# Kernel optimization log

Hardware: AMD Instinct MI355X
Metric: run time of the kernel (lower is better)

Reference implementation:

```python
import jax, jax.numpy as jnp
import numpy as np

HEADS = 16
DIM_HEAD = 64
NEG_INF = -1e30


def _rope_cos_sin(seq_len, dim_head, dtype):
    inv_freq = 1.0 / (10000.0 ** (jnp.arange(0, dim_head, 2, dtype=jnp.float32) / dim_head))
    t = jnp.arange(seq_len, dtype=jnp.float32)
    freqs = jnp.einsum('i,j->ij', t, inv_freq)          # [n, dh/2]
    emb = jnp.concatenate([freqs, freqs], axis=-1)       # [n, dh]
    return jnp.cos(emb).astype(dtype), jnp.sin(emb).astype(dtype)


def _rotate_half(x):
    x1, x2 = jnp.split(x, 2, axis=-1)
    return jnp.concatenate([-x2, x1], axis=-1)


def setup_inputs() -> dict:
    key = jax.random.key(0)
    k1, k2, k3 = jax.random.split(key, 3)
    dim = HEADS * DIM_HEAD  # 1024
    x = jax.random.normal(k1, (2, 2048, dim), dtype=jnp.float32)
    w_qkv = jax.random.normal(k2, (dim, 3 * dim), dtype=jnp.float32) * (dim ** -0.5)
    w_out = jax.random.normal(k3, (dim, dim), dtype=jnp.float32) * (dim ** -0.5)
    return {"x": x, "w_qkv": w_qkv, "w_out": w_out}


def reference(x, w_qkv, w_out):
    b, n, d = x.shape
    h, dh = HEADS, DIM_HEAD
    scale = dh ** -0.5

    qkv = x @ w_qkv                                      # [b, n, 3*h*dh]
    q, k, v = jnp.split(qkv, 3, axis=-1)
    reshape = lambda t: t.reshape(b, n, h, dh).transpose(0, 2, 1, 3)  # b h n dh
    q, k, v = reshape(q), reshape(k), reshape(v)

    cos, sin = _rope_cos_sin(n, dh, x.dtype)
    cos = cos[None, None, :, :]
    sin = sin[None, None, :, :]
    q = q * cos + _rotate_half(q) * sin
    k = k * cos + _rotate_half(k) * sin

    scores = jnp.einsum('bhid,bhjd->bhij', q, k) * scale  # [b, h, n, n]
    causal = jnp.triu(jnp.ones((n, n), dtype=bool), k=1)
    scores = jnp.where(causal[None, None, :, :], NEG_INF, scores)
    attn = jax.nn.softmax(scores, axis=-1)

    out = jnp.einsum('bhij,bhjd->bhid', attn, v)          # [b, h, n, dh]
    out = out.transpose(0, 2, 1, 3).reshape(b, n, h * dh)
    return out @ w_out
```

## Files before the change

kernel.cpp:

```cpp
#include <hip/hip_runtime.h>

#define SEQ 2048
#define NH 16
#define DH 64
#define DMODEL 1024
#define NQKV 3072

typedef __attribute__((ext_vector_type(8))) short bf16x8;
typedef __attribute__((ext_vector_type(4))) short bf16x4;
typedef __attribute__((ext_vector_type(4))) float f32x4;

#define GLOAD16(src, dst)                                                              \
  __builtin_amdgcn_global_load_lds((const __attribute__((address_space(1))) void*)(src), \
                                   (__attribute__((address_space(3))) void*)(dst), 16, 0, 0)

__device__ __forceinline__ unsigned short f2bf(float f) {
  union { float f; unsigned u; } v; v.f = f;
  unsigned r = v.u + 0x7FFFu + ((v.u >> 16) & 1u);
  return (unsigned short)(r >> 16);
}

__device__ __forceinline__ unsigned pkbf(float a, float b) {
  unsigned r;
  asm("v_cvt_pk_bf16_f32 %0, %1, %2" : "=v"(r) : "v"(a), "v"(b));
  return r;
}

__device__ __forceinline__ void transw_body(const float* __restrict__ in,
                                            unsigned short* __restrict__ out,
                                            int K, int N, int k0, int n0, int tid,
                                            float (*Ts)[65]) {
#pragma unroll
  for (int p = 0; p < 4; ++p) {
    int id = p * 256 + tid;
    int r = id >> 4, c4 = (id & 15) * 4;
    const f32x4 v = *reinterpret_cast<const f32x4*>(&in[(size_t)(k0 + r) * N + n0 + c4]);
    Ts[r][c4] = v[0]; Ts[r][c4 + 1] = v[1]; Ts[r][c4 + 2] = v[2]; Ts[r][c4 + 3] = v[3];
  }
  __syncthreads();
#pragma unroll
  for (int p = 0; p < 2; ++p) {
    int id = p * 256 + tid;
    int n = id >> 3, k8 = (id & 7) * 8;
    unsigned short tmp[8];
#pragma unroll
    for (int i = 0; i < 8; ++i) tmp[i] = f2bf(Ts[k8 + i][n]);
    *reinterpret_cast<bf16x8*>(&out[(size_t)(n0 + n) * K + k0 + k8]) =
        *reinterpret_cast<bf16x8*>(tmp);
  }
}

__global__ __launch_bounds__(256) void prep_kernel(
    const float* __restrict__ x, const float* __restrict__ w_qkv,
    const float* __restrict__ w_out, unsigned short* __restrict__ Xb,
    unsigned short* __restrict__ WqkvT, unsigned short* __restrict__ WoutT,
    float* __restrict__ cost, float* __restrict__ sint) {
  __shared__ float Ts[64][65];
  const int tid = threadIdx.x;
  const int id = blockIdx.x;
  if (id < 2048) {
    int idx = id * 256 + tid;
    const f32x4 v0 = *reinterpret_cast<const f32x4*>(&x[(size_t)idx * 8]);
    const f32x4 v1 = *reinterpret_cast<const f32x4*>(&x[(size_t)idx * 8 + 4]);
    bf16x8 o;
    o[0] = (short)f2bf(v0[0]); o[1] = (short)f2bf(v0[1]);
    o[2] = (short)f2bf(v0[2]); o[3] = (short)f2bf(v0[3]);
    o[4] = (short)f2bf(v1[0]); o[5] = (short)f2bf(v1[1]);
    o[6] = (short)f2bf(v1[2]); o[7] = (short)f2bf(v1[3]);
    *reinterpret_cast<bf16x8*>(&Xb[(size_t)idx * 8]) = o;
  } else if (id < 2816) {
    int t = id - 2048;
    transw_body(w_qkv, WqkvT, DMODEL, NQKV, (t & 15) * 64, (t >> 4) * 64, tid, Ts);
  } else if (id < 3072) {
    int t = id - 2816;
    transw_body(w_out, WoutT, DMODEL, DMODEL, (t & 15) * 64, (t >> 4) * 64, tid, Ts);
  } else {
    int idx = (id - 3072) * 256 + tid;
    int t = idx >> 5, j = idx & 31;
    float inv = powf(10000.0f, -(float)(2 * j) / 64.0f);
    float a = (float)t * inv;
    cost[idx] = cosf(a);
    sint[idx] = sinf(a);
  }
}

__global__ __launch_bounds__(256) void gemm_qkv_kernel(
    const unsigned short* __restrict__ Xb, const unsigned short* __restrict__ BT,
    unsigned short* __restrict__ Qb, unsigned short* __restrict__ Kb,
    unsigned short* __restrict__ Vtg,
    const float* __restrict__ cost, const float* __restrict__ sint) {
  __shared__ unsigned short As[3][4096];
  __shared__ unsigned short Bs[3][4096];

  const int tid = threadIdx.x;
  const int lane = tid & 63;
  const int w = tid >> 6;
  const int lam = lane & 15;
  const int g = lane >> 4;
  const int wr = w >> 1, wc = w & 1;
  const int rowBase = blockIdx.x * 128;
  const int colBase = blockIdx.y * 128;

  f32x4 acc[4][4];
#pragma unroll
  for (int m = 0; m < 4; ++m)
#pragma unroll
    for (int n = 0; n < 4; ++n) acc[m][n] = (f32x4){0.f, 0.f, 0.f, 0.f};

#define GSTAGE(buf, kk0)                                                               \
  {                                                                                    \
    _Pragma("unroll") for (int c = 0; c < 2; ++c) {                                    \
      int ch = c * 256 + w * 64 + lane;                                                \
      int row = ch >> 2, q = ch & 3;                                                   \
      GLOAD16(Xb + (size_t)(rowBase + row) * DMODEL + (kk0) + ((q ^ (row & 3)) * 8),   \
              &As[buf][0] + (c * 256 + w * 64) * 8);                                   \
      GLOAD16(BT + (size_t)(colBase + row) * DMODEL + (kk0) + ((q ^ (row & 3)) * 8),   \
              &Bs[buf][0] + (c * 256 + w * 64) * 8);                                   \
    }                                                                                  \
  }

  GSTAGE(0, 0);
  GSTAGE(1, 32);

  for (int kb = 0; kb < 32; ++kb) {
    if (kb + 2 < 32) {
      GSTAGE((kb + 2) % 3, (kb + 2) * 32);
      asm volatile("s_waitcnt vmcnt(8)" ::: "memory");
    } else if (kb + 1 < 32) {
      asm volatile("s_waitcnt vmcnt(4)" ::: "memory");
    } else {
      asm volatile("s_waitcnt vmcnt(0)" ::: "memory");
    }
    __builtin_amdgcn_s_barrier();
    const int cb = kb % 3;
    bf16x8 a[4], b[4];
    const int sw = (g ^ (lam & 3)) * 8;
#pragma unroll
    for (int m = 0; m < 4; ++m)
      a[m] = *reinterpret_cast<bf16x8*>(&As[cb][(wr * 64 + m * 16 + lam) * 32 + sw]);
#pragma unroll
    for (int n = 0; n < 4; ++n)
      b[n] = *reinterpret_cast<bf16x8*>(&Bs[cb][(wc * 64 + n * 16 + lam) * 32 + sw]);
    __builtin_amdgcn_s_setprio(1);
#pragma unroll
    for (int m = 0; m < 4; ++m)
#pragma unroll
      for (int n = 0; n < 4; ++n)
        acc[m][n] = __builtin_amdgcn_mfma_f32_16x16x32_bf16(a[m], b[n], acc[m][n], 0, 0, 0);
    __builtin_amdgcn_s_setprio(0);
    asm volatile("s_waitcnt lgkmcnt(0)" ::: "memory");
    __builtin_amdgcn_s_barrier();
  }
#undef GSTAGE

  const int mat = blockIdx.y >> 3;
  if (mat < 2) {
    unsigned short* dst = mat ? Kb : Qb;
    const float sc = mat ? 1.0f : 0.125f;
    const int h = ((colBase & 1023) + wc * 64) >> 6;
#pragma unroll
    for (int m = 0; m < 4; ++m) {
#pragma unroll
      for (int r = 0; r < 4; ++r) {
        int row = rowBase + wr * 64 + m * 16 + g * 4 + r;
        int bi = row >> 11, t = row & 2047;
        unsigned short* out = &dst[(size_t)((bi * NH + h) * SEQ + t) * DH];
#pragma unroll
        for (int n = 0; n < 2; ++n) {
          int j = n * 16 + lam;
          float c = cost[t * 32 + j], s = sint[t * 32 + j];
          float x0 = acc[m][n][r], x1 = acc[m][n + 2][r];
          out[j] = f2bf((x0 * c - x1 * s) * sc);
          out[j + 32] = f2bf((x1 * c + x0 * s) * sc);
        }
      }
    }
  } else {
    unsigned short (*Vbuf)[44] = reinterpret_cast<unsigned short(*)[44]>(&As[0][0]);
    const int b = rowBase >> 11, t0 = rowBase & 2047;
#pragma unroll
    for (int cc = 0; cc < 4; ++cc) {
      __syncthreads();
      if (wc == (cc >> 1)) {
        const int n0 = (cc & 1) * 2;
#pragma unroll
        for (int m = 0; m < 4; ++m)
#pragma unroll
          for (int r = 0; r < 4; ++r)
#pragma unroll
            for (int n2 = 0; n2 < 2; ++n2)
              Vbuf[wr * 64 + m * 16 + g * 4 + r][n2 * 16 + lam] = f2bf(acc[m][n0 + n2][r]);
      }
      __syncthreads();
      const int colq0 = colBase - 2048 + cc * 32;
#pragma unroll
      for (int p2 = 0; p2 < 2; ++p2) {
        int ch = p2 * 256 + tid;
        int d = ch & 31, tq = (ch >> 5) * 8;
        unsigned short tmp[8];
#pragma unroll
        for (int i = 0; i < 8; ++i) tmp[i] = Vbuf[tq + i][d];
        int col = colq0 + d;
        int h = col >> 6, dd = col & 63;
        *reinterpret_cast<bf16x8*>(&Vtg[((size_t)(b * NH + h) * DH + dd) * SEQ + t0 + tq]) =
            *reinterpret_cast<bf16x8*>(tmp);
      }
    }
  }
}

__global__ __launch_bounds__(256) void attn_kernel(
    const unsigned short* __restrict__ Qb, const unsigned short* __restrict__ Kb,
    const unsigned short* __restrict__ Vtg, unsigned short* __restrict__ Ob) {
  __shared__ unsigned short Ks[2][8192];
  __shared__ unsigned short Vs[2][8192];
  __shared__ unsigned short Ps[4][2048];

  const int tid = threadIdx.x;
  const int lane = tid & 63;
  const int w = tid >> 6;
  const int lam = lane & 15;
  const int g = lane >> 4;
  const int bh = blockIdx.x;
  const int p = blockIdx.y;
  const int qtA = p, qtB = 31 - p;
  const int nA = (p >> 1) + 1;
  const int nB = ((31 - p) >> 1) + 1;
  const int nT = nA + nB;
  const int ql = w * 16 + lam;

  const unsigned short* kallbase = Kb + (size_t)bh * SEQ * DH;
  const unsigned short* vallbase = Vtg + (size_t)bh * DH * SEQ;

  bf16x8 qb0, qb1;
  f32x4 oacc[4], sa0[4], sa1[4];
  float mr, lr;

#define LOADQ(qt)                                                                     \
  {                                                                                   \
    const unsigned short* qrow = Qb + ((size_t)bh * SEQ + (qt) * 64 + w * 16 + lam) * DH; \
    qb0 = *reinterpret_cast<const bf16x8*>(&qrow[g * 8]);                             \
    qb1 = *reinterpret_cast<const bf16x8*>(&qrow[g * 8 + 32]);                        \
  }
#define RESET_STATE()                                                                 \
  {                                                                                   \
    _Pragma("unroll") for (int f = 0; f < 4; ++f) oacc[f] = (f32x4){0.f, 0.f, 0.f, 0.f}; \
    mr = -1e30f; lr = 0.f;                                                            \
  }
#define STAGE(buf, jt)                                                                \
  {                                                                                   \
    const unsigned short* kb2 = kallbase + (size_t)(jt) * 128 * DH;                   \
    const unsigned short* vb2 = vallbase + (size_t)(jt) * 128;                        \
    _Pragma("unroll") for (int c = 0; c < 4; ++c) {                                   \
      int id = c * 256 + w * 64 + lane;                                               \
      int kr = id >> 3, kq = id & 7;                                                  \
      GLOAD16(kb2 + kr * DH + ((kq ^ (kr & 7)) * 8), &Ks[buf][0] + id * 8);           \
      int vr = id >> 4, vq = id & 15;                                                 \
      GLOAD16(vb2 + (size_t)vr * SEQ + ((vq ^ (vr & 15)) * 8), &Vs[buf][0] + id * 8); \
    }                                                                                 \
  }
#define FLUSHO(qt)                                                                    \
  {                                                                                   \
    const int b = bh >> 4, h = bh & 15;                                               \
    float rinv = 1.0f / lr;                                                           \
    _Pragma("unroll") for (int r = 0; r < 4; ++r) {                                   \
      int n = (qt) * 64 + w * 16 + g * 4 + r;                                         \
      float inv = __shfl(rinv, g * 4 + r);                                            \
      unsigned short* orow = &Ob[(size_t)(b * SEQ + n) * DMODEL + h * DH];            \
      _Pragma("unroll") for (int f = 0; f < 4; ++f) orow[f * 16 + lam] = f2bf(oacc[f][r] * inv); \
    }                                                                                 \
  }

  RESET_STATE();
  LOADQ(qtA);
  STAGE(0, 0);
  asm volatile("s_waitcnt vmcnt(0)" ::: "memory");
  __syncthreads();

  int cur = 0;
  for (int i = 0; i < nT; ++i) {
    const int onA = (i < nA);
    const int qt = onA ? qtA : qtB;
    const int j = onA ? i : (i - nA);

    if (i + 1 < nT) {
      const int jn = (i + 1 < nA) ? (i + 1) : (i + 1 - nA);
      STAGE(cur ^ 1, jn);
    }

    const int t1 = 2 * j + 1;
    const bool diag0 = (2 * j == qt);
    const bool diag1 = (t1 == qt);
    const bool skip1 = (t1 > qt);

#pragma unroll
    for (int f = 0; f < 4; ++f) {
      sa0[f] = (f32x4){0.f, 0.f, 0.f, 0.f};
      sa1[f] = (f32x4){0.f, 0.f, 0.f, 0.f};
    }
    __builtin_amdgcn_s_setprio(1);
#pragma unroll
    for (int f = 0; f < 4; ++f) {
      int kr = f * 16 + lam;
      bf16x8 k0 = *reinterpret_cast<bf16x8*>(&Ks[cur][kr * 64 + ((g ^ (kr & 7)) * 8)]);
      bf16x8 k1 = *reinterpret_cast<bf16x8*>(&Ks[cur][kr * 64 + (((g + 4) ^ (kr & 7)) * 8)]);
      sa0[f] = __builtin_amdgcn_mfma_f32_16x16x32_bf16(k0, qb0, sa0[f], 0, 0, 0);
      sa0[f] = __builtin_amdgcn_mfma_f32_16x16x32_bf16(k1, qb1, sa0[f], 0, 0, 0);
    }
    if (!skip1) {
#pragma unroll
      for (int f = 0; f < 4; ++f) {
        int kr = 64 + f * 16 + lam;
        bf16x8 k0 = *reinterpret_cast<bf16x8*>(&Ks[cur][kr * 64 + ((g ^ (kr & 7)) * 8)]);
        bf16x8 k1 = *reinterpret_cast<bf16x8*>(&Ks[cur][kr * 64 + (((g + 4) ^ (kr & 7)) * 8)]);
        sa1[f] = __builtin_amdgcn_mfma_f32_16x16x32_bf16(k0, qb0, sa1[f], 0, 0, 0);
        sa1[f] = __builtin_amdgcn_mfma_f32_16x16x32_bf16(k1, qb1, sa1[f], 0, 0, 0);
      }
    }
    __builtin_amdgcn_s_setprio(0);

    if (diag0) {
#pragma unroll
      for (int f = 0; f < 4; ++f)
#pragma unroll
        for (int r = 0; r < 4; ++r)
          if (f * 16 + g * 4 + r > ql) sa0[f][r] = -1e30f;
    }
    if (diag1) {
#pragma unroll
      for (int f = 0; f < 4; ++f)
#pragma unroll
        for (int r = 0; r < 4; ++r)
          if (f * 16 + g * 4 + r > ql) sa1[f][r] = -1e30f;
    }

    float mx = -1e30f;
#pragma unroll
    for (int f = 0; f < 4; ++f)
#pragma unroll
      for (int r = 0; r < 4; ++r) mx = fmaxf(mx, sa0[f][r]);
    if (!skip1) {
#pragma unroll
      for (int f = 0; f < 4; ++f)
#pragma unroll
        for (int r = 0; r < 4; ++r) mx = fmaxf(mx, sa1[f][r]);
    }
    mx = fmaxf(mx, __shfl_xor(mx, 16));
    mx = fmaxf(mx, __shfl_xor(mx, 32));
    float mn = fmaxf(mr, mx);
    float alpha = __expf(mr - mn);
    mr = mn;

    float sum = 0.f;
#pragma unroll
    for (int f = 0; f < 4; ++f)
#pragma unroll
      for (int r = 0; r < 4; ++r) {
        sa0[f][r] = __expf(sa0[f][r] - mn);
        sum += sa0[f][r];
      }
    if (!skip1) {
#pragma unroll
      for (int f = 0; f < 4; ++f)
#pragma unroll
        for (int r = 0; r < 4; ++r) {
          sa1[f][r] = __expf(sa1[f][r] - mn);
          sum += sa1[f][r];
        }
    }
    sum += __shfl_xor(sum, 16);
    sum += __shfl_xor(sum, 32);
    lr = lr * alpha + sum;

#pragma unroll
    for (int r = 0; r < 4; ++r) {
      float af = __shfl(alpha, g * 4 + r);
#pragma unroll
      for (int f = 0; f < 4; ++f) oacc[f][r] *= af;
    }

#pragma unroll
    for (int f = 0; f < 4; ++f) {
      uint2 u;
      u.x = pkbf(sa0[f][0], sa0[f][1]);
      u.y = pkbf(sa0[f][2], sa0[f][3]);
      int chunk = f * 2 + (g >> 1);
      *reinterpret_cast<uint2*>(
          &Ps[w][lam * 128 + ((chunk ^ (lam & 15)) * 8) + ((g & 1) * 4)]) = u;
    }
    if (!skip1) {
#pragma unroll
      for (int f = 0; f < 4; ++f) {
        uint2 u;
        u.x = pkbf(sa1[f][0], sa1[f][1]);
        u.y = pkbf(sa1[f][2], sa1[f][3]);
        int chunk = 8 + f * 2 + (g >> 1);
        *reinterpret_cast<uint2*>(
            &Ps[w][lam * 128 + ((chunk ^ (lam & 15)) * 8) + ((g & 1) * 4)]) = u;
      }
    }

    bf16x8 pa0 = *reinterpret_cast<bf16x8*>(&Ps[w][lam * 128 + ((g ^ (lam & 15)) * 8)]);
    bf16x8 pa1 = *reinterpret_cast<bf16x8*>(&Ps[w][lam * 128 + (((4 + g) ^ (lam & 15)) * 8)]);
    __builtin_amdgcn_s_setprio(1);
#pragma unroll
    for (int f = 0; f < 4; ++f) {
      int vr = f * 16 + lam;
      bf16x8 v0 = *reinterpret_cast<bf16x8*>(&Vs[cur][vr * 128 + ((g ^ (vr & 15)) * 8)]);
      bf16x8 v1 = *reinterpret_cast<bf16x8*>(&Vs[cur][vr * 128 + (((4 + g) ^ (vr & 15)) * 8)]);
      oacc[f] = __builtin_amdgcn_mfma_f32_16x16x32_bf16(pa0, v0, oacc[f], 0, 0, 0);
      oacc[f] = __builtin_amdgcn_mfma_f32_16x16x32_bf16(pa1, v1, oacc[f], 0, 0, 0);
    }
    __builtin_amdgcn_s_setprio(0);
    if (!skip1) {
      bf16x8 pa2 = *reinterpret_cast<bf16x8*>(&Ps[w][lam * 128 + (((8 + g) ^ (lam & 15)) * 8)]);
      bf16x8 pa3 = *reinterpret_cast<bf16x8*>(&Ps[w][lam * 128 + (((12 + g) ^ (lam & 15)) * 8)]);
      __builtin_amdgcn_s_setprio(1);
#pragma unroll
      for (int f = 0; f < 4; ++f) {
        int vr = f * 16 + lam;
        bf16x8 v2 = *reinterpret_cast<bf16x8*>(&Vs[cur][vr * 128 + (((8 + g) ^ (vr & 15)) * 8)]);
        bf16x8 v3 = *reinterpret_cast<bf16x8*>(&Vs[cur][vr * 128 + (((12 + g) ^ (vr & 15)) * 8)]);
        oacc[f] = __builtin_amdgcn_mfma_f32_16x16x32_bf16(pa2, v2, oacc[f], 0, 0, 0);
        oacc[f] = __builtin_amdgcn_mfma_f32_16x16x32_bf16(pa3, v3, oacc[f], 0, 0, 0);
      }
      __builtin_amdgcn_s_setprio(0);
    }

    if (i == nA - 1) {
      FLUSHO(qtA);
      RESET_STATE();
      LOADQ(qtB);
    }

    asm volatile("s_waitcnt vmcnt(0)" ::: "memory");
    __syncthreads();
    cur ^= 1;
  }
  FLUSHO(qtB);
#undef LOADQ
#undef RESET_STATE
#undef STAGE
#undef FLUSHO
}

__global__ __launch_bounds__(256) void gemm_out_kernel(
    const unsigned short* __restrict__ A, const unsigned short* __restrict__ BT,
    float* __restrict__ C) {
  __shared__ unsigned short As[3][4096];
  __shared__ unsigned short Bs[3][4096];

  const int tid = threadIdx.x;
  const int lane = tid & 63;
  const int w = tid >> 6;
  const int lam = lane & 15;
  const int g = lane >> 4;
  const int wr = w >> 1, wc = w & 1;
  const int rowBase = blockIdx.x * 128;
  const int colBase = blockIdx.y * 128;

  f32x4 acc[4][4];
#pragma unroll
  for (int m = 0; m < 4; ++m)
#pragma unroll
    for (int n = 0; n < 4; ++n) acc[m][n] = (f32x4){0.f, 0.f, 0.f, 0.f};

#define GSTAGE(buf, kk0)                                                               \
  {                                                                                    \
    _Pragma("unroll") for (int c = 0; c < 2; ++c) {                                    \
      int ch = c * 256 + w * 64 + lane;                                                \
      int row = ch >> 2, q = ch & 3;                                                   \
      GLOAD16(A + (size_t)(rowBase + row) * DMODEL + (kk0) + ((q ^ (row & 3)) * 8),    \
              &As[buf][0] + (c * 256 + w * 64) * 8);                                   \
      GLOAD16(BT + (size_t)(colBase + row) * DMODEL + (kk0) + ((q ^ (row & 3)) * 8),   \
              &Bs[buf][0] + (c * 256 + w * 64) * 8);                                   \
    }                                                                                  \
  }

  GSTAGE(0, 0);
  GSTAGE(1, 32);

  for (int kb = 0; kb < 32; ++kb) {
    if (kb + 2 < 32) {
      GSTAGE((kb + 2) % 3, (kb + 2) * 32);
      asm volatile("s_waitcnt vmcnt(8)" ::: "memory");
    } else if (kb + 1 < 32) {
      asm volatile("s_waitcnt vmcnt(4)" ::: "memory");
    } else {
      asm volatile("s_waitcnt vmcnt(0)" ::: "memory");
    }
    __builtin_amdgcn_s_barrier();
    const int cb = kb % 3;
    bf16x8 a[4], b[4];
    const int sw = (g ^ (lam & 3)) * 8;
#pragma unroll
    for (int m = 0; m < 4; ++m)
      a[m] = *reinterpret_cast<bf16x8*>(&As[cb][(wr * 64 + m * 16 + lam) * 32 + sw]);
#pragma unroll
    for (int n = 0; n < 4; ++n)
      b[n] = *reinterpret_cast<bf16x8*>(&Bs[cb][(wc * 64 + n * 16 + lam) * 32 + sw]);
    __builtin_amdgcn_s_setprio(1);
#pragma unroll
    for (int m = 0; m < 4; ++m)
#pragma unroll
      for (int n = 0; n < 4; ++n)
        acc[m][n] = __builtin_amdgcn_mfma_f32_16x16x32_bf16(a[m], b[n], acc[m][n], 0, 0, 0);
    __builtin_amdgcn_s_setprio(0);
    asm volatile("s_waitcnt lgkmcnt(0)" ::: "memory");
    __builtin_amdgcn_s_barrier();
  }
#undef GSTAGE

#pragma unroll
  for (int m = 0; m < 4; ++m)
#pragma unroll
    for (int r = 0; r < 4; ++r) {
      int row = rowBase + wr * 64 + m * 16 + g * 4 + r;
#pragma unroll
      for (int n = 0; n < 4; ++n)
        C[(size_t)row * DMODEL + colBase + wc * 64 + n * 16 + lam] = acc[m][n][r];
    }
}

extern "C" void kernel_launch(void* const* d_in, const int* in_sizes, int n_in,
                              void* d_out, int out_size, void* d_ws, size_t ws_size,
                              hipStream_t stream) {
  const float* x = (const float*)d_in[0];
  const float* w_qkv = (const float*)d_in[1];
  const float* w_out = (const float*)d_in[2];
  float* out = (float*)d_out;

  char* ws = (char*)d_ws;
  const size_t MB = 1024 * 1024;
  unsigned short* WqkvT = (unsigned short*)(ws);
  float* cost = (float*)(ws + 6 * MB);
  float* sint = cost + SEQ * 32;
  unsigned short* Ob = (unsigned short*)(ws);
  unsigned short* WoutT = (unsigned short*)(ws + 8 * MB);
  unsigned short* Qb = (unsigned short*)(ws + 10 * MB);
  unsigned short* Kb = (unsigned short*)(ws + 18 * MB);
  unsigned short* Vtg = (unsigned short*)(ws + 26 * MB);
  unsigned short* Xb = (unsigned short*)d_out;

  prep_kernel<<<3328, 256, 0, stream>>>(x, w_qkv, w_out, Xb, WqkvT, WoutT, cost, sint);
  gemm_qkv_kernel<<<dim3(32, 24), 256, 0, stream>>>(Xb, WqkvT, Qb, Kb, Vtg, cost, sint);
  attn_kernel<<<dim3(32, 16), 256, 0, stream>>>(Qb, Kb, Vtg, Ob);
  gemm_out_kernel<<<dim3(32, 8), 256, 0, stream>>>(Ob, WoutT, out);
}
```

Measured before the change: 133.0 us.

## Restructure attention to 128-row query tiles with direct global K/V loads

```diff
diff --git a/kernel.cpp b/kernel.cpp
--- a/kernel.cpp
+++ b/kernel.cpp
@@ -212,9 +212,7 @@
 __global__ __launch_bounds__(256) void attn_kernel(
     const unsigned short* __restrict__ Qb, const unsigned short* __restrict__ Kb,
     const unsigned short* __restrict__ Vtg, unsigned short* __restrict__ Ob) {
-  __shared__ unsigned short Ks[2][8192];
-  __shared__ unsigned short Vs[2][8192];
-  __shared__ unsigned short Ps[4][2048];
+  __shared__ unsigned short Ps[4][32 * 128];
 
   const int tid = threadIdx.x;
   const int lane = tid & 63;
@@ -223,207 +221,151 @@
   const int g = lane >> 4;
   const int bh = blockIdx.x;
   const int p = blockIdx.y;
-  const int qtA = p, qtB = 31 - p;
-  const int nA = (p >> 1) + 1;
-  const int nB = ((31 - p) >> 1) + 1;
-  const int nT = nA + nB;
-  const int ql = w * 16 + lam;
-
-  const unsigned short* kallbase = Kb + (size_t)bh * SEQ * DH;
-  const unsigned short* vallbase = Vtg + (size_t)bh * DH * SEQ;
-
-  bf16x8 qb0, qb1;
-  f32x4 oacc[4], sa0[4], sa1[4];
-  float mr, lr;
-
-#define LOADQ(qt)                                                                     \
-  {                                                                                   \
-    const unsigned short* qrow = Qb + ((size_t)bh * SEQ + (qt) * 64 + w * 16 + lam) * DH; \
-    qb0 = *reinterpret_cast<const bf16x8*>(&qrow[g * 8]);                             \
-    qb1 = *reinterpret_cast<const bf16x8*>(&qrow[g * 8 + 32]);                        \
-  }
-#define RESET_STATE()                                                                 \
-  {                                                                                   \
-    _Pragma("unroll") for (int f = 0; f < 4; ++f) oacc[f] = (f32x4){0.f, 0.f, 0.f, 0.f}; \
-    mr = -1e30f; lr = 0.f;                                                            \
-  }
-#define STAGE(buf, jt)                                                                \
-  {                                                                                   \
-    const unsigned short* kb2 = kallbase + (size_t)(jt) * 128 * DH;                   \
-    const unsigned short* vb2 = vallbase + (size_t)(jt) * 128;                        \
-    _Pragma("unroll") for (int c = 0; c < 4; ++c) {                                   \
-      int id = c * 256 + w * 64 + lane;                                               \
-      int kr = id >> 3, kq = id & 7;                                                  \
-      GLOAD16(kb2 + kr * DH + ((kq ^ (kr & 7)) * 8), &Ks[buf][0] + id * 8);           \
-      int vr = id >> 4, vq = id & 15;                                                 \
-      GLOAD16(vb2 + (size_t)vr * SEQ + ((vq ^ (vr & 15)) * 8), &Vs[buf][0] + id * 8); \
-    }                                                                                 \
-  }
-#define FLUSHO(qt)                                                                    \
-  {                                                                                   \
-    const int b = bh >> 4, h = bh & 15;                                               \
-    float rinv = 1.0f / lr;                                                           \
-    _Pragma("unroll") for (int r = 0; r < 4; ++r) {                                   \
-      int n = (qt) * 64 + w * 16 + g * 4 + r;                                         \
-      float inv = __shfl(rinv, g * 4 + r);                                            \
-      unsigned short* orow = &Ob[(size_t)(b * SEQ + n) * DMODEL + h * DH];            \
-      _Pragma("unroll") for (int f = 0; f < 4; ++f) orow[f * 16 + lam] = f2bf(oacc[f][r] * inv); \
-    }                                                                                 \
+  const int qtA = p, qtB = 15 - p;
+  const int nA = p + 1;
+  const int nT = 17;
+
+  const unsigned short* kall = Kb + (size_t)bh * SEQ * DH;
+  const unsigned short* vall = Vtg + (size_t)bh * DH * SEQ;
+
+  bf16x8 qb[2][2];
+  f32x4 oacc[2][4];
+  float mr[2], lr[2];
+
+#define LOADQ(qt)                                                                      \
+  {                                                                                    \
+    _Pragma("unroll") for (int m = 0; m < 2; ++m) {                                    \
+      const unsigned short* qrow =                                                     \
+          Qb + ((size_t)bh * SEQ + (qt) * 128 + w * 32 + m * 16 + lam) * DH;           \
+      qb[m][0] = *reinterpret_cast<const bf16x8*>(&qrow[g * 8]);                       \
+      qb[m][1] = *reinterpret_cast<const bf16x8*>(&qrow[g * 8 + 32]);                  \
+    }                                                                                  \
+  }
+#define RESET_STATE()                                                                  \
+  {                                                                                    \
+    _Pragma("unroll") for (int m = 0; m < 2; ++m) {                                    \
+      _Pragma("unroll") for (int f = 0; f < 4; ++f) oacc[m][f] = (f32x4){0.f, 0.f, 0.f, 0.f}; \
+      mr[m] = -1e30f; lr[m] = 0.f;                                                     \
+    }                                                                                  \
+  }
+#define FLUSHO(qt)                                                                     \
+  {                                                                                    \
+    const int b = bh >> 4, h = bh & 15;                                                \
+    _Pragma("unroll") for (int m = 0; m < 2; ++m) {                                    \
+      float rinv = 1.0f / lr[m];                                                       \
+      _Pragma("unroll") for (int r = 0; r < 4; ++r) {                                  \
+        int n = (qt) * 128 + w * 32 + m * 16 + g * 4 + r;                              \
+        float inv = __shfl(rinv, g * 4 + r);                                           \
+        unsigned short* orow = &Ob[(size_t)(b * SEQ + n) * DMODEL + h * DH];           \
+        _Pragma("unroll") for (int f = 0; f < 4; ++f)                                  \
+            orow[f * 16 + lam] = f2bf(oacc[m][f][r] * inv);                            \
+      }                                                                                \
+    }                                                                                  \
   }
 
   RESET_STATE();
   LOADQ(qtA);
-  STAGE(0, 0);
-  asm volatile("s_waitcnt vmcnt(0)" ::: "memory");
-  __syncthreads();
-
-  int cur = 0;
+
   for (int i = 0; i < nT; ++i) {
     const int onA = (i < nA);
     const int qt = onA ? qtA : qtB;
     const int j = onA ? i : (i - nA);
-
-    if (i + 1 < nT) {
-      const int jn = (i + 1 < nA) ? (i + 1) : (i + 1 - nA);
-      STAGE(cur ^ 1, jn);
-    }
-
-    const int t1 = 2 * j + 1;
-    const bool diag0 = (2 * j == qt);
-    const bool diag1 = (t1 == qt);
-    const bool skip1 = (t1 > qt);
-
+    const unsigned short* kb2 = kall + (size_t)j * 128 * DH;
+    const unsigned short* vb2 = vall + (size_t)j * 128;
+
+    f32x4 sac[2][8];
+#pragma unroll
+    for (int m = 0; m < 2; ++m)
+#pragma unroll
+      for (int f = 0; f < 8; ++f) sac[m][f] = (f32x4){0.f, 0.f, 0.f, 0.f};
+#pragma unroll
+    for (int f = 0; f < 8; ++f) {
+      const unsigned short* krow = kb2 + (f * 16 + lam) * DH;
+      bf16x8 k0 = *reinterpret_cast<const bf16x8*>(&krow[g * 8]);
+      bf16x8 k1 = *reinterpret_cast<const bf16x8*>(&krow[32 + g * 8]);
+      __builtin_amdgcn_s_setprio(1);
+#pragma unroll
+      for (int m = 0; m < 2; ++m) {
+        sac[m][f] = __builtin_amdgcn_mfma_f32_16x16x32_bf16(k0, qb[m][0], sac[m][f], 0, 0, 0);
+        sac[m][f] = __builtin_amdgcn_mfma_f32_16x16x32_bf16(k1, qb[m][1], sac[m][f], 0, 0, 0);
+      }
+      __builtin_amdgcn_s_setprio(0);
+    }
+
+    if (j == qt) {
+#pragma unroll
+      for (int m = 0; m < 2; ++m) {
+        const int ql = w * 32 + m * 16 + lam;
+#pragma unroll
+        for (int f = 0; f < 8; ++f)
+#pragma unroll
+          for (int r = 0; r < 4; ++r)
+            if (f * 16 + g * 4 + r > ql) sac[m][f][r] = -1e30f;
+      }
+    }
+
+#pragma unroll
+    for (int m = 0; m < 2; ++m) {
+      float mx = -1e30f;
+#pragma unroll
+      for (int f = 0; f < 8; ++f)
+#pragma unroll
+        for (int r = 0; r < 4; ++r) mx = fmaxf(mx, sac[m][f][r]);
+      mx = fmaxf(mx, __shfl_xor(mx, 16));
+      mx = fmaxf(mx, __shfl_xor(mx, 32));
+      float mn = fmaxf(mr[m], mx);
+      float alpha = __expf(mr[m] - mn);
+      mr[m] = mn;
+      float sum = 0.f;
+#pragma unroll
+      for (int f = 0; f < 8; ++f)
+#pragma unroll
+        for (int r = 0; r < 4; ++r) {
+          sac[m][f][r] = __expf(sac[m][f][r] - mn);
+          sum += sac[m][f][r];
+        }
+      sum += __shfl_xor(sum, 16);
+      sum += __shfl_xor(sum, 32);
+      lr[m] = lr[m] * alpha + sum;
+#pragma unroll
+      for (int r = 0; r < 4; ++r) {
+        float af = __shfl(alpha, g * 4 + r);
+#pragma unroll
+        for (int f = 0; f < 4; ++f) oacc[m][f][r] *= af;
+      }
+      const int row = m * 16 + lam;
+#pragma unroll
+      for (int f = 0; f < 8; ++f) {
+        uint2 u;
+        u.x = pkbf(sac[m][f][0], sac[m][f][1]);
+        u.y = pkbf(sac[m][f][2], sac[m][f][3]);
+        int chunk = f * 2 + (g >> 1);
+        *reinterpret_cast<uint2*>(
+            &Ps[w][row * 128 + ((chunk ^ lam) * 8) + ((g & 1) * 4)]) = u;
+      }
+    }
+
+    bf16x8 pa[2][4];
+#pragma unroll
+    for (int m = 0; m < 2; ++m) {
+      const int row = m * 16 + lam;
+#pragma unroll
+      for (int ks = 0; ks < 4; ++ks)
+        pa[m][ks] = *reinterpret_cast<bf16x8*>(&Ps[w][row * 128 + (((ks * 4 + g) ^ lam) * 8)]);
+    }
 #pragma unroll
     for (int f = 0; f < 4; ++f) {
-      sa0[f] = (f32x4){0.f, 0.f, 0.f, 0.f};
-      sa1[f] = (f32x4){0.f, 0.f, 0.f, 0.f};
-    }
-    __builtin_amdgcn_s_setprio(1);
-#pragma unroll
-    for (int f = 0; f < 4; ++f) {
-      int kr = f * 16 + lam;
-      bf16x8 k0 = *reinterpret_cast<bf16x8*>(&Ks[cur][kr * 64 + ((g ^ (kr & 7)) * 8)]);
-      bf16x8 k1 = *reinterpret_cast<bf16x8*>(&Ks[cur][kr * 64 + (((g + 4) ^ (kr & 7)) * 8)]);
-      sa0[f] = __builtin_amdgcn_mfma_f32_16x16x32_bf16(k0, qb0, sa0[f], 0, 0, 0);
-      sa0[f] = __builtin_amdgcn_mfma_f32_16x16x32_bf16(k1, qb1, sa0[f], 0, 0, 0);
-    }
-    if (!skip1) {
-#pragma unroll
-      for (int f = 0; f < 4; ++f) {
-        int kr = 64 + f * 16 + lam;
-        bf16x8 k0 = *reinterpret_cast<bf16x8*>(&Ks[cur][kr * 64 + ((g ^ (kr & 7)) * 8)]);
-        bf16x8 k1 = *reinterpret_cast<bf16x8*>(&Ks[cur][kr * 64 + (((g + 4) ^ (kr & 7)) * 8)]);
-        sa1[f] = __builtin_amdgcn_mfma_f32_16x16x32_bf16(k0, qb0, sa1[f], 0, 0, 0);
-        sa1[f] = __builtin_amdgcn_mfma_f32_16x16x32_bf16(k1, qb1, sa1[f], 0, 0, 0);
-      }
-    }
-    __builtin_amdgcn_s_setprio(0);
-
-    if (diag0) {
-#pragma unroll
-      for (int f = 0; f < 4; ++f)
-#pragma unroll
-        for (int r = 0; r < 4; ++r)
-          if (f * 16 + g * 4 + r > ql) sa0[f][r] = -1e30f;
-    }
-    if (diag1) {
-#pragma unroll
-      for (int f = 0; f < 4; ++f)
-#pragma unroll
-        for (int r = 0; r < 4; ++r)
-          if (f * 16 + g * 4 + r > ql) sa1[f][r] = -1e30f;
-    }
-
-    float mx = -1e30f;
-#pragma unroll
-    for (int f = 0; f < 4; ++f)
-#pragma unroll
-      for (int r = 0; r < 4; ++r) mx = fmaxf(mx, sa0[f][r]);
-    if (!skip1) {
-#pragma unroll
-      for (int f = 0; f < 4; ++f)
-#pragma unroll
-        for (int r = 0; r < 4; ++r) mx = fmaxf(mx, sa1[f][r]);
-    }
-    mx = fmaxf(mx, __shfl_xor(mx, 16));
-    mx = fmaxf(mx, __shfl_xor(mx, 32));
-    float mn = fmaxf(mr, mx);
-    float alpha = __expf(mr - mn);
-    mr = mn;
-
-    float sum = 0.f;
-#pragma unroll
-    for (int f = 0; f < 4; ++f)
-#pragma unroll
-      for (int r = 0; r < 4; ++r) {
-        sa0[f][r] = __expf(sa0[f][r] - mn);
-        sum += sa0[f][r];
-      }
-    if (!skip1) {
-#pragma unroll
-      for (int f = 0; f < 4; ++f)
-#pragma unroll
-        for (int r = 0; r < 4; ++r) {
-          sa1[f][r] = __expf(sa1[f][r] - mn);
-          sum += sa1[f][r];
-        }
-    }
-    sum += __shfl_xor(sum, 16);
-    sum += __shfl_xor(sum, 32);
-    lr = lr * alpha + sum;
-
-#pragma unroll
-    for (int r = 0; r < 4; ++r) {
-      float af = __shfl(alpha, g * 4 + r);
-#pragma unroll
-      for (int f = 0; f < 4; ++f) oacc[f][r] *= af;
-    }
-
-#pragma unroll
-    for (int f = 0; f < 4; ++f) {
-      uint2 u;
-      u.x = pkbf(sa0[f][0], sa0[f][1]);
-      u.y = pkbf(sa0[f][2], sa0[f][3]);
-      int chunk = f * 2 + (g >> 1);
-      *reinterpret_cast<uint2*>(
-          &Ps[w][lam * 128 + ((chunk ^ (lam & 15)) * 8) + ((g & 1) * 4)]) = u;
-    }
-    if (!skip1) {
-#pragma unroll
-      for (int f = 0; f < 4; ++f) {
-        uint2 u;
-        u.x = pkbf(sa1[f][0], sa1[f][1]);
-        u.y = pkbf(sa1[f][2], sa1[f][3]);
-        int chunk = 8 + f * 2 + (g >> 1);
-        *reinterpret_cast<uint2*>(
-            &Ps[w][lam * 128 + ((chunk ^ (lam & 15)) * 8) + ((g & 1) * 4)]) = u;
-      }
-    }
-
-    bf16x8 pa0 = *reinterpret_cast<bf16x8*>(&Ps[w][lam * 128 + ((g ^ (lam & 15)) * 8)]);
-    bf16x8 pa1 = *reinterpret_cast<bf16x8*>(&Ps[w][lam * 128 + (((4 + g) ^ (lam & 15)) * 8)]);
-    __builtin_amdgcn_s_setprio(1);
-#pragma unroll
-    for (int f = 0; f < 4; ++f) {
-      int vr = f * 16 + lam;
-      bf16x8 v0 = *reinterpret_cast<bf16x8*>(&Vs[cur][vr * 128 + ((g ^ (vr & 15)) * 8)]);
-      bf16x8 v1 = *reinterpret_cast<bf16x8*>(&Vs[cur][vr * 128 + (((4 + g) ^ (vr & 15)) * 8)]);
-      oacc[f] = __builtin_amdgcn_mfma_f32_16x16x32_bf16(pa0, v0, oacc[f], 0, 0, 0);
-      oacc[f] = __builtin_amdgcn_mfma_f32_16x16x32_bf16(pa1, v1, oacc[f], 0, 0, 0);
-    }
-    __builtin_amdgcn_s_setprio(0);
-    if (!skip1) {
-      bf16x8 pa2 = *reinterpret_cast<bf16x8*>(&Ps[w][lam * 128 + (((8 + g) ^ (lam & 15)) * 8)]);
-      bf16x8 pa3 = *reinterpret_cast<bf16x8*>(&Ps[w][lam * 128 + (((12 + g) ^ (lam & 15)) * 8)]);
+      const unsigned short* vrow = vb2 + (size_t)(f * 16 + lam) * SEQ;
+      bf16x8 vv[4];
+#pragma unroll
+      for (int ks = 0; ks < 4; ++ks)
+        vv[ks] = *reinterpret_cast<const bf16x8*>(&vrow[ks * 32 + g * 8]);
       __builtin_amdgcn_s_setprio(1);
 #pragma unroll
-      for (int f = 0; f < 4; ++f) {
-        int vr = f * 16 + lam;
-        bf16x8 v2 = *reinterpret_cast<bf16x8*>(&Vs[cur][vr * 128 + (((8 + g) ^ (vr & 15)) * 8)]);
-        bf16x8 v3 = *reinterpret_cast<bf16x8*>(&Vs[cur][vr * 128 + (((12 + g) ^ (vr & 15)) * 8)]);
-        oacc[f] = __builtin_amdgcn_mfma_f32_16x16x32_bf16(pa2, v2, oacc[f], 0, 0, 0);
-        oacc[f] = __builtin_amdgcn_mfma_f32_16x16x32_bf16(pa3, v3, oacc[f], 0, 0, 0);
-      }
+      for (int m = 0; m < 2; ++m)
+#pragma unroll
+        for (int ks = 0; ks < 4; ++ks)
+          oacc[m][f] = __builtin_amdgcn_mfma_f32_16x16x32_bf16(pa[m][ks], vv[ks], oacc[m][f], 0, 0, 0);
       __builtin_amdgcn_s_setprio(0);
     }
 
@@ -432,15 +374,10 @@
       RESET_STATE();
       LOADQ(qtB);
     }
-
-    asm volatile("s_waitcnt vmcnt(0)" ::: "memory");
-    __syncthreads();
-    cur ^= 1;
   }
   FLUSHO(qtB);
 #undef LOADQ
 #undef RESET_STATE
-#undef STAGE
 #undef FLUSHO
 }
 
@@ -544,6 +481,6 @@
 
   prep_kernel<<<3328, 256, 0, stream>>>(x, w_qkv, w_out, Xb, WqkvT, WoutT, cost, sint);
   gemm_qkv_kernel<<<dim3(32, 24), 256, 0, stream>>>(Xb, WqkvT, Qb, Kb, Vtg, cost, sint);
-  attn_kernel<<<dim3(32, 16), 256, 0, stream>>>(Qb, Kb, Vtg, Ob);
+  attn_kernel<<<dim3(32, 8), 256, 0, stream>>>(Qb, Kb, Vtg, Ob);
   gemm_out_kernel<<<dim3(32, 8), 256, 0, stream>>>(Ob, WoutT, out);
 }
```

New measurement: 175.3 us. 31.8% more time.
